# Performance work log

Measured on AMD Instinct MI355X. Metric: run time of the kernel, lower is better.

Reference implementation:

```python
import jax, jax.numpy as jnp
from jax import lax
import numpy as np

SIGMAS = (30.0, 150.0, 300.0)
RESTORE_FACTOR = 2.0
COLOR_GAIN = 10.0
GAIN = 270.0
OFFSET = 128.0
EPS = 1e-6


def _dwconv(x, k2d, stride):
    # depthwise 2D conv, NCHW, VALID padding (caller pads)
    C = x.shape[1]
    kh, kw = k2d.shape
    w = jnp.broadcast_to(k2d.astype(x.dtype)[None, None], (C, 1, kh, kw))
    return lax.conv_general_dilated(
        x, w, (stride, stride), 'VALID',
        dimension_numbers=('NCHW', 'OIHW', 'NCHW'),
        feature_group_count=C)


def _pyr_down(x):
    # cv2.pyrDown: 5x5 binomial kernel, reflect-101 border, stride-2 decimation
    k1 = jnp.array([1., 4., 6., 4., 1.], jnp.float32) / 16.0
    k2 = jnp.outer(k1, k1)
    xp = jnp.pad(x, ((0, 0), (0, 0), (2, 2), (2, 2)), mode='reflect')
    return _dwconv(xp, k2, 2)


def _gauss_blur(x, ksize):
    # cv2.GaussianBlur with sigmaX=0: sigma derived from kernel size
    s = 0.3 * ((ksize - 1) * 0.5 - 1.0) + 0.8
    i = jnp.arange(ksize, dtype=jnp.float32) - (ksize - 1) / 2.0
    g = jnp.exp(-(i * i) / (2.0 * s * s))
    g = g / g.sum()
    k2 = jnp.outer(g, g)
    p = ksize // 2
    xp = jnp.pad(x, ((0, 0), (0, 0), (p, p), (p, p)), mode='reflect')
    return _dwconv(xp, k2, 1)


def _fast_filter(x, sigma):
    # Faithful port of GaussianBlurConv.FastFilter (static Python recursion:
    # sigma is a compile-time constant, so depth is fixed at trace time).
    sigma = min(sigma, 300.0)
    k = int(round(sigma * 3 * 2 + 1)) | 1
    if k < 3:
        return x
    if k < 10:
        return _gauss_blur(x, k)
    h, w = x.shape[2], x.shape[3]
    if h < 2 or w < 2:
        return x
    sub = _fast_filter(_pyr_down(x), sigma / 2.0)
    # cv2.resize default INTER_LINEAR == half-pixel bilinear
    return jax.image.resize(sub, (x.shape[0], x.shape[1], h, w), method='bilinear')


def _msr_forward(x):
    img = x * 255.0 + 1.0                      # (N,3,H,W)
    log_img = jnp.log10(img + EPS)
    retinex = sum(log_img - jnp.log10(_fast_filter(img, s) + EPS) for s in SIGMAS)
    retinex = retinex / len(SIGMAS)
    img_sum = jnp.sum(img, axis=1, keepdims=True)   # (N,1,H,W)
    color_rest = jnp.log10(img * RESTORE_FACTOR / (img_sum + EPS) + 1.0)
    enhanced = retinex * color_rest * COLOR_GAIN * GAIN + OFFSET
    return jnp.clip(enhanced, 0.0, 255.0) / 255.0


def setup_inputs() -> dict:
    key = jax.random.key(0)
    x = jax.random.uniform(key, (8, 3, 1280, 1280), dtype=jnp.float32)
    return {"x": x}


def reference(x):
    return _msr_forward(x)
```

## Files before the change

kernel.cpp:

```cpp
#include <hip/hip_runtime.h>

#define NC 24

typedef float f32x4 __attribute__((ext_vector_type(4)));

__device__ __forceinline__ float pyr_point(const float* ip, int Hi, int Wi, int oy, int ox)
{
    const float k1[5] = {0.0625f, 0.25f, 0.375f, 0.25f, 0.0625f};
    float acc = 0.f;
#pragma unroll
    for (int i = 0; i < 5; ++i) {
        int y = 2 * oy - 2 + i;
        y = (y < 0) ? -y : y;
        y = (y >= Hi) ? (2 * Hi - 2 - y) : y;
        const float* rp = ip + (size_t)y * Wi;
        float r = 0.f;
#pragma unroll
        for (int j = 0; j < 5; ++j) {
            int xx = 2 * ox - 2 + j;
            xx = (xx < 0) ? -xx : xx;
            xx = (xx >= Wi) ? (2 * Wi - 2 - xx) : xx;
            r = fmaf(k1[j], rp[xx], r);
        }
        acc = fmaf(k1[i], r, acc);
    }
    return acc;
}

template <int K>
__device__ __forceinline__ float blur_point(const float* ip, int H, int W, int oy, int ox,
                                            const float* w)
{
    const int R = K / 2;
    float acc = 0.f;
#pragma unroll
    for (int i = 0; i < K; ++i) {
        int y = oy - R + i;
        y = (y < 0) ? -y : y;
        y = (y >= H) ? (2 * H - 2 - y) : y;
        const float* rp = ip + (size_t)y * W;
        float r = 0.f;
#pragma unroll
        for (int j = 0; j < K; ++j) {
            int xx = ox - R + j;
            xx = (xx < 0) ? -xx : xx;
            xx = (xx >= W) ? (2 * W - 2 - xx) : xx;
            r = fmaf(w[j], rp[xx], r);
        }
        acc = fmaf(w[i], r, acc);
    }
    return acc;
}

template <int HI, int WI>
__global__ void __launch_bounds__(256) pyrdown_v2(
    const float* __restrict__ in, float* __restrict__ out, float scale, float offs)
{
    const int HO = HI / 2, WO = WI / 2;
    __shared__ float tile[35][136];
    __shared__ float vs[16][132];
    const int tid = threadIdx.x;
    const int OX = blockIdx.x * 64;
    const int OY = blockIdx.y * 16;
    const int nc = blockIdx.z;
    const float k1[5] = {0.0625f, 0.25f, 0.375f, 0.25f, 0.0625f};
    const float* ip = in + (size_t)nc * HI * WI;
    const int gx0 = 2 * OX - 4;

    if (gx0 >= 0 && gx0 + 135 < WI) {
        for (int v = tid; v < 35 * 34; v += 256) {
            int r = v / 34, q = v - r * 34;
            int y = 2 * OY - 2 + r;
            y = (y < 0) ? -y : y;
            y = (y >= HI) ? (2 * HI - 2 - y) : y;
            *(f32x4*)&tile[r][4 * q] = *(const f32x4*)&ip[(size_t)y * WI + gx0 + 4 * q];
        }
    } else {
        for (int v = tid; v < 35 * 136; v += 256) {
            int r = v / 136, c = v - r * 136;
            int y = 2 * OY - 2 + r;
            y = (y < 0) ? -y : y;
            y = (y >= HI) ? (2 * HI - 2 - y) : y;
            y = min(max(y, 0), HI - 1);
            int x = gx0 + c;
            x = (x < 0) ? -x : x;
            x = (x >= WI) ? (2 * WI - 2 - x) : x;
            x = min(max(x, 0), WI - 1);
            tile[r][c] = ip[(size_t)y * WI + x];
        }
    }
    __syncthreads();

    for (int v = tid; v < 16 * 132; v += 256) {
        int r = v / 132, c = v - r * 132;
        float acc = k1[0] * tile[2 * r][c + 2];
#pragma unroll
        for (int i = 1; i < 5; ++i) acc = fmaf(k1[i], tile[2 * r + i][c + 2], acc);
        vs[r][c] = acc;
    }
    __syncthreads();

    for (int o = tid; o < 1024; o += 256) {
        int r = o >> 6, c = o & 63;
        int ox = OX + c, oy = OY + r;
        if (ox >= WO || oy >= HO) continue;
        float acc = k1[0] * vs[r][2 * c];
#pragma unroll
        for (int j = 1; j < 5; ++j) acc = fmaf(k1[j], vs[r][2 * c + j], acc);
        out[((size_t)nc * HO + oy) * WO + ox] = fmaf(acc, scale, offs);
    }
}

__global__ void __launch_bounds__(512) base_kernel(
    const float* __restrict__ L4g, float* __restrict__ b30g,
    float* __restrict__ b150g, float* __restrict__ b300g)
{
    __shared__ float sL4[80 * 80];
    __shared__ float sL5[40 * 40];
    __shared__ float sL6[20 * 20];
    __shared__ float sL7[10 * 10];
    __shared__ float sL8[5 * 5];
    const int nc = blockIdx.x;
    const int tid = threadIdx.x;

    float w7[7], w9[9];
    {
        float s = 1.4f, s2 = 2.f * s * s, sum = 0.f;
#pragma unroll
        for (int i = 0; i < 7; ++i) { float d = (float)i - 3.f; w7[i] = expf(-(d * d) / s2); sum += w7[i]; }
#pragma unroll
        for (int i = 0; i < 7; ++i) w7[i] /= sum;
        s = 1.7f; s2 = 2.f * s * s; sum = 0.f;
#pragma unroll
        for (int i = 0; i < 9; ++i) { float d = (float)i - 4.f; w9[i] = expf(-(d * d) / s2); sum += w9[i]; }
#pragma unroll
        for (int i = 0; i < 9; ++i) w9[i] /= sum;
    }

    const float* src = L4g + (size_t)nc * 6400;
    for (int i = tid; i < 1600; i += 512)
        *(f32x4*)&sL4[4 * i] = *(const f32x4*)&src[4 * i];
    __syncthreads();
    for (int i = tid; i < 1600; i += 512) {
        int oy = i / 40, ox = i - oy * 40;
        sL5[i] = pyr_point(sL4, 80, 80, oy, ox);
    }
    __syncthreads();
    for (int i = tid; i < 400; i += 512) {
        int oy = i / 20, ox = i - oy * 20;
        sL6[i] = pyr_point(sL5, 40, 40, oy, ox);
    }
    __syncthreads();
    for (int i = tid; i < 100; i += 512) {
        int oy = i / 10, ox = i - oy * 10;
        sL7[i] = pyr_point(sL6, 20, 20, oy, ox);
    }
    __syncthreads();
    for (int i = tid; i < 25; i += 512) {
        int oy = i / 5, ox = i - oy * 5;
        sL8[i] = pyr_point(sL7, 10, 10, oy, ox);
    }
    __syncthreads();
    for (int i = tid; i < 1600; i += 512) {
        int oy = i / 40, ox = i - oy * 40;
        b30g[(size_t)nc * 1600 + i] = blur_point<7>(sL5, 40, 40, oy, ox, w7);
    }
    for (int i = tid; i < 100; i += 512) {
        int oy = i / 10, ox = i - oy * 10;
        b150g[(size_t)nc * 100 + i] = blur_point<9>(sL7, 10, 10, oy, ox, w9);
    }
    for (int i = tid; i < 25; i += 512) {
        int oy = i / 5, ox = i - oy * 5;
        b300g[(size_t)nc * 25 + i] = blur_point<9>(sL8, 5, 5, oy, ox, w9);
    }
}

#define CH 1721
#define O30_3 0
#define O30_2 36
#define O30_1 100
#define O30_0 244
#define O150_5 568
#define O150_4 593
#define O150_3 618
#define O150_2 654
#define O150_1 718
#define O150_0 862
#define O300_6 1186
#define O300_5 1211
#define O300_4 1236
#define O300_3 1261
#define O300_2 1297
#define O300_1 1333
#define O300_0 1397

template <int NPL, int ND, int NS, int LSD>
__device__ __forceinline__ void up_level(float* __restrict__ S,
                                         const int (&srcO)[NPL], const int (&dstO)[NPL],
                                         int ayD, int axD, int ayS, int axS)
{
    const int SSRC = LSD / 2;
    const int NPTS = ND * ND;
    for (int pt = threadIdx.x; pt < NPTS; pt += 256) {
        int ry = pt / ND, rx = pt - ry * ND;
        int gy = min(max(ayD + ry, 0), LSD - 1);
        int gx = min(max(axD + rx, 0), LSD - 1);
        int my = gy >> 1, py = gy & 1;
        int mx = gx >> 1, px = gx & 1;
        int yA = py ? my : max(my - 1, 0);
        int yB = py ? min(my + 1, SSRC - 1) : my;
        float wyA = py ? 0.75f : 0.25f;
        float wyB = 1.0f - wyA;
        int xA = px ? mx : max(mx - 1, 0);
        int xB = px ? min(mx + 1, SSRC - 1) : mx;
        float wxA = px ? 0.75f : 0.25f;
        float wxB = 1.0f - wxA;
        int la = (yA - ayS) * NS + (xA - axS);
        int laB = la + (xB - xA);
        int lb = (yB - ayS) * NS + (xA - axS);
        int lbB = lb + (xB - xA);
#pragma unroll
        for (int p = 0; p < NPL; ++p) {
            const float* sp = S + srcO[p];
            float v = wyA * fmaf(wxA, sp[la], wxB * sp[laB]) +
                      wyB * fmaf(wxA, sp[lb], wxB * sp[lbB]);
            S[dstO[p] + pt] = v;
        }
    }
}

__global__ void __launch_bounds__(256) mega_final(
    const float* __restrict__ x,
    const float* __restrict__ b30g,
    const float* __restrict__ b150g,
    const float* __restrict__ b300g,
    float* __restrict__ out)
{
    const int H = 1280, W = 1280;
    __shared__ float S[3 * CH];

    const int tid = threadIdx.x;
    const int X0 = blockIdx.x * 64, Y0 = blockIdx.y * 64;
    const int n = blockIdx.z;

    int ay[7], ax[7];
    ay[0] = (Y0 >> 2) - 1;
    ax[0] = (X0 >> 2) - 1;
#pragma unroll
    for (int l = 1; l < 7; ++l) {
        ay[l] = (ay[l - 1] >> 1) - 1;
        ax[l] = (ax[l - 1] >> 1) - 1;
    }

    if (tid < 36) {
        int ry = tid / 6, rx = tid - ry * 6;
        int gy = min(max(ay[3] + ry, 0), 39);
        int gx = min(max(ax[3] + rx, 0), 39);
#pragma unroll
        for (int c = 0; c < 3; ++c)
            S[c * CH + O30_3 + tid] = b30g[(size_t)(n * 3 + c) * 1600 + gy * 40 + gx];
    } else if (tid >= 64 && tid < 89) {
        int t = tid - 64;
        int ry = t / 5, rx = t - ry * 5;
        int gy = min(max(ay[5] + ry, 0), 9);
        int gx = min(max(ax[5] + rx, 0), 9);
#pragma unroll
        for (int c = 0; c < 3; ++c)
            S[c * CH + O150_5 + t] = b150g[(size_t)(n * 3 + c) * 100 + gy * 10 + gx];
    } else if (tid >= 128 && tid < 153) {
        int t = tid - 128;
        int ry = t / 5, rx = t - ry * 5;
        int gy = min(max(ay[6] + ry, 0), 4);
        int gx = min(max(ax[6] + rx, 0), 4);
#pragma unroll
        for (int c = 0; c < 3; ++c)
            S[c * CH + O300_6 + t] = b300g[(size_t)(n * 3 + c) * 25 + gy * 5 + gx];
    }
    __syncthreads();

    {
        const int s[3] = {O300_6, O300_6 + CH, O300_6 + 2 * CH};
        const int d[3] = {O300_5, O300_5 + CH, O300_5 + 2 * CH};
        up_level<3, 5, 5, 10>(S, s, d, ay[5], ax[5], ay[6], ax[6]);
    }
    __syncthreads();
    {
        const int s[6] = {O300_5, O300_5 + CH, O300_5 + 2 * CH, O150_5, O150_5 + CH, O150_5 + 2 * CH};
        const int d[6] = {O300_4, O300_4 + CH, O300_4 + 2 * CH, O150_4, O150_4 + CH, O150_4 + 2 * CH};
        up_level<6, 5, 5, 20>(S, s, d, ay[4], ax[4], ay[5], ax[5]);
    }
    __syncthreads();
    {
        const int s[6] = {O300_4, O300_4 + CH, O300_4 + 2 * CH, O150_4, O150_4 + CH, O150_4 + 2 * CH};
        const int d[6] = {O300_3, O300_3 + CH, O300_3 + 2 * CH, O150_3, O150_3 + CH, O150_3 + 2 * CH};
        up_level<6, 6, 5, 40>(S, s, d, ay[3], ax[3], ay[4], ax[4]);
    }
    __syncthreads();
    {
        const int s[9] = {O300_3, O300_3 + CH, O300_3 + 2 * CH, O150_3, O150_3 + CH, O150_3 + 2 * CH,
                          O30_3, O30_3 + CH, O30_3 + 2 * CH};
        const int d[9] = {O300_2, O300_2 + CH, O300_2 + 2 * CH, O150_2, O150_2 + CH, O150_2 + 2 * CH,
                          O30_2, O30_2 + CH, O30_2 + 2 * CH};
        up_level<9, 8, 6, 80>(S, s, d, ay[2], ax[2], ay[3], ax[3]);
    }
    __syncthreads();
    {
        const int s[9] = {O300_2, O300_2 + CH, O300_2 + 2 * CH, O150_2, O150_2 + CH, O150_2 + 2 * CH,
                          O30_2, O30_2 + CH, O30_2 + 2 * CH};
        const int d[9] = {O300_1, O300_1 + CH, O300_1 + 2 * CH, O150_1, O150_1 + CH, O150_1 + 2 * CH,
                          O30_1, O30_1 + CH, O30_1 + 2 * CH};
        up_level<9, 12, 8, 160>(S, s, d, ay[1], ax[1], ay[2], ax[2]);
    }
    __syncthreads();
    {
        const int s[9] = {O300_1, O300_1 + CH, O300_1 + 2 * CH, O150_1, O150_1 + CH, O150_1 + 2 * CH,
                          O30_1, O30_1 + CH, O30_1 + 2 * CH};
        const int d[9] = {O300_0, O300_0 + CH, O300_0 + 2 * CH, O150_0, O150_0 + CH, O150_0 + 2 * CH,
                          O30_0, O30_0 + CH, O30_0 + 2 * CH};
        up_level<9, 18, 12, 320>(S, s, d, ay[0], ax[0], ay[1], ax[1]);
    }
    __syncthreads();

    int tyi = tid >> 4, txi = tid & 15;
    int byi = (Y0 >> 2) + tyi, bxi = (X0 >> 2) + txi;
    int ry[3], rx[3];
    ry[0] = max(byi - 1, 0) - ay[0]; ry[1] = byi - ay[0]; ry[2] = min(byi + 1, 319) - ay[0];
    rx[0] = max(bxi - 1, 0) - ax[0]; rx[1] = bxi - ax[0]; rx[2] = min(bxi + 1, 319) - ax[0];
    const int ol0[3] = {O30_0, O150_0, O300_0};

    f32x4 xi[3][4];
#pragma unroll
    for (int c = 0; c < 3; ++c)
#pragma unroll
        for (int qy = 0; qy < 4; ++qy)
            xi[c][qy] = __builtin_nontemporal_load(
                (const f32x4*)&x[((size_t)(n * 3 + c) * H + 4 * byi + qy) * W + 4 * bxi]);

    float crcp[4][4];
#pragma unroll
    for (int qy = 0; qy < 4; ++qy)
#pragma unroll
        for (int qx = 0; qx < 4; ++qx) {
            float s = (xi[0][qy][qx] + xi[1][qy][qx] + xi[2][qy][qx]) * 255.f + 3.f;
            crcp[qy][qx] = __fdividef(2.f, s + 1e-6f);
        }

#pragma unroll
    for (int c = 0; c < 3; ++c) {
        float prod[4][4];
#pragma unroll
        for (int qy = 0; qy < 4; ++qy)
#pragma unroll
            for (int qx = 0; qx < 4; ++qx) prod[qy][qx] = 1.f;

#pragma unroll
        for (int s = 0; s < 3; ++s) {
            const float* fp = &S[c * CH + ol0[s]];
            float v[3][3];
#pragma unroll
            for (int i = 0; i < 3; ++i)
#pragma unroll
                for (int j = 0; j < 3; ++j) v[i][j] = fp[ry[i] * 18 + rx[j]];
            float cy[4][3];
#pragma unroll
            for (int j = 0; j < 3; ++j) {
                float v0 = v[0][j], v1 = v[1][j], v2 = v[2][j];
                cy[0][j] = fmaf(0.375f, v0, 0.625f * v1);
                cy[1][j] = fmaf(0.1875f, v0, fmaf(0.75f, v1, 0.0625f * v2));
                cy[2][j] = fmaf(0.0625f, v0, fmaf(0.75f, v1, 0.1875f * v2));
                cy[3][j] = fmaf(0.625f, v1, 0.375f * v2);
            }
#pragma unroll
            for (int qy = 0; qy < 4; ++qy) {
                float a0 = cy[qy][0], a1 = cy[qy][1], a2 = cy[qy][2];
                float t0 = fmaf(0.375f, a0, 0.625f * a1);
                float t1 = fmaf(0.1875f, a0, fmaf(0.75f, a1, 0.0625f * a2));
                float t2 = fmaf(0.0625f, a0, fmaf(0.75f, a1, 0.1875f * a2));
                float t3 = fmaf(0.625f, a1, 0.375f * a2);
                prod[qy][0] *= (t0 + 1e-6f);
                prod[qy][1] *= (t1 + 1e-6f);
                prod[qy][2] *= (t2 + 1e-6f);
                prod[qy][3] *= (t3 + 1e-6f);
            }
        }

#pragma unroll
        for (int qy = 0; qy < 4; ++qy) {
            f32x4 o;
#pragma unroll
            for (int qx = 0; qx < 4; ++qx) {
                float img = xi[c][qy][qx] * 255.f + 1.f;
                float a = img + 1e-6f;
                float l2a = __log2f(__fdividef(a * a * a, prod[qy][qx]));
                float carg = fmaf(img, crcp[qy][qx], 1.f);
                float l2c = __log2f(carg);
                float e = fmaf(l2a * l2c, 81.55715246f, 128.f);
                e = fminf(fmaxf(e, 0.f), 255.f);
                o[qx] = e * (1.f / 255.f);
            }
            __builtin_nontemporal_store(
                o, (f32x4*)&out[((size_t)(n * 3 + c) * H + 4 * byi + qy) * W + 4 * bxi]);
        }
    }
}

extern "C" void kernel_launch(void* const* d_in, const int* in_sizes, int n_in,
                              void* d_out, int out_size, void* d_ws, size_t ws_size,
                              hipStream_t stream)
{
    const float* x = (const float*)d_in[0];
    float* out = (float*)d_out;
    float* ws = (float*)d_ws;

    size_t off = 0;
    auto alloc = [&](int d) { float* p = ws + off; off += (size_t)NC * d * d; return p; };
    float* L1 = alloc(640);
    float* L2 = alloc(320);
    float* L3 = alloc(160);
    float* L4 = alloc(80);
    float* b30 = alloc(40);
    float* b150 = alloc(10);
    float* b300 = alloc(5);
    (void)ws_size; (void)in_sizes; (void)n_in; (void)out_size;

    dim3 blk(256, 1, 1);

    pyrdown_v2<1280, 1280><<<dim3(10, 40, NC), blk, 0, stream>>>(x,  L1, 255.f, 1.f);
    pyrdown_v2<640, 640><<<dim3(5, 20, NC), blk, 0, stream>>>(L1, L2, 1.f, 0.f);
    pyrdown_v2<320, 320><<<dim3(3, 10, NC), blk, 0, stream>>>(L2, L3, 1.f, 0.f);
    pyrdown_v2<160, 160><<<dim3(2, 5, NC), blk, 0, stream>>>(L3, L4, 1.f, 0.f);
    base_kernel<<<dim3(NC, 1, 1), dim3(512, 1, 1), 0, stream>>>(L4, b30, b150, b300);
    mega_final<<<dim3(20, 20, 8), dim3(256, 1, 1), 0, stream>>>(x, b30, b150, b300, out);
}
```

Baseline: 351.5 us.

## Collapse cascaded bilinear upsampling into precomputed separable 3-tap weights

The chain of per-level bilinear upsample stages in shared memory, each followed by a barrier, is replaced by a direct mapping from a 3x3 coarse-level neighbourhood to each output pixel. The mapping uses separable weights that are computed per row and column once per block by composing the linear interpolation steps. This removes six barriers and the intermediate shared-memory levels, and shrinks the shared-memory footprint. In exchange each thread does more FMAs per pixel, loads weights from shared memory, and keeps more live registers (prod for all three channels). Accuracy relies on the composed weights matching the clamped border behaviour of the original cascade.

```diff
diff --git a/kernel.cpp b/kernel.cpp
--- a/kernel.cpp
+++ b/kernel.cpp
@@ -175,60 +175,6 @@
     }
 }
 
-#define CH 1721
-#define O30_3 0
-#define O30_2 36
-#define O30_1 100
-#define O30_0 244
-#define O150_5 568
-#define O150_4 593
-#define O150_3 618
-#define O150_2 654
-#define O150_1 718
-#define O150_0 862
-#define O300_6 1186
-#define O300_5 1211
-#define O300_4 1236
-#define O300_3 1261
-#define O300_2 1297
-#define O300_1 1333
-#define O300_0 1397
-
-template <int NPL, int ND, int NS, int LSD>
-__device__ __forceinline__ void up_level(float* __restrict__ S,
-                                         const int (&srcO)[NPL], const int (&dstO)[NPL],
-                                         int ayD, int axD, int ayS, int axS)
-{
-    const int SSRC = LSD / 2;
-    const int NPTS = ND * ND;
-    for (int pt = threadIdx.x; pt < NPTS; pt += 256) {
-        int ry = pt / ND, rx = pt - ry * ND;
-        int gy = min(max(ayD + ry, 0), LSD - 1);
-        int gx = min(max(axD + rx, 0), LSD - 1);
-        int my = gy >> 1, py = gy & 1;
-        int mx = gx >> 1, px = gx & 1;
-        int yA = py ? my : max(my - 1, 0);
-        int yB = py ? min(my + 1, SSRC - 1) : my;
-        float wyA = py ? 0.75f : 0.25f;
-        float wyB = 1.0f - wyA;
-        int xA = px ? mx : max(mx - 1, 0);
-        int xB = px ? min(mx + 1, SSRC - 1) : mx;
-        float wxA = px ? 0.75f : 0.25f;
-        float wxB = 1.0f - wxA;
-        int la = (yA - ayS) * NS + (xA - axS);
-        int laB = la + (xB - xA);
-        int lb = (yB - ayS) * NS + (xA - axS);
-        int lbB = lb + (xB - xA);
-#pragma unroll
-        for (int p = 0; p < NPL; ++p) {
-            const float* sp = S + srcO[p];
-            float v = wyA * fmaf(wxA, sp[la], wxB * sp[laB]) +
-                      wyB * fmaf(wxA, sp[lb], wxB * sp[lbB]);
-            S[dstO[p] + pt] = v;
-        }
-    }
-}
-
 __global__ void __launch_bounds__(256) mega_final(
     const float* __restrict__ x,
     const float* __restrict__ b30g,
@@ -237,96 +183,104 @@
     float* __restrict__ out)
 {
     const int H = 1280, W = 1280;
-    __shared__ float S[3 * CH];
+    __shared__ float W30[32][3];
+    __shared__ float W150[128][3];
+    __shared__ float W300[256][3];
+    __shared__ float P30[3][4][4];
+    __shared__ float P150[3][3][3];
+    __shared__ float P300[3][3][3];
 
     const int tid = threadIdx.x;
-    const int X0 = blockIdx.x * 64, Y0 = blockIdx.y * 64;
-    const int n = blockIdx.z;
-
-    int ay[7], ax[7];
-    ay[0] = (Y0 >> 2) - 1;
-    ax[0] = (X0 >> 2) - 1;
-#pragma unroll
-    for (int l = 1; l < 7; ++l) {
-        ay[l] = (ay[l - 1] >> 1) - 1;
-        ax[l] = (ax[l - 1] >> 1) - 1;
-    }
-
-    if (tid < 36) {
-        int ry = tid / 6, rx = tid - ry * 6;
-        int gy = min(max(ay[3] + ry, 0), 39);
-        int gx = min(max(ax[3] + rx, 0), 39);
-#pragma unroll
-        for (int c = 0; c < 3; ++c)
-            S[c * CH + O30_3 + tid] = b30g[(size_t)(n * 3 + c) * 1600 + gy * 40 + gx];
-    } else if (tid >= 64 && tid < 89) {
-        int t = tid - 64;
-        int ry = t / 5, rx = t - ry * 5;
-        int gy = min(max(ay[5] + ry, 0), 9);
-        int gx = min(max(ax[5] + rx, 0), 9);
-#pragma unroll
-        for (int c = 0; c < 3; ++c)
-            S[c * CH + O150_5 + t] = b150g[(size_t)(n * 3 + c) * 100 + gy * 10 + gx];
-    } else if (tid >= 128 && tid < 153) {
-        int t = tid - 128;
-        int ry = t / 5, rx = t - ry * 5;
-        int gy = min(max(ay[6] + ry, 0), 4);
-        int gx = min(max(ax[6] + rx, 0), 4);
-#pragma unroll
-        for (int c = 0; c < 3; ++c)
-            S[c * CH + O300_6 + t] = b300g[(size_t)(n * 3 + c) * 25 + gy * 5 + gx];
-    }
-    __syncthreads();
+    const int bx = blockIdx.x, by = blockIdx.y, n = blockIdx.z;
+
+    for (int r = tid; r < 416; r += 256) {
+        int idx, nst; float* dst;
+        if (r < 32)       { idx = r;       nst = 5; dst = W30[r]; }
+        else if (r < 160) { idx = r - 32;  nst = 7; dst = W150[r - 32]; }
+        else              { idx = r - 160; nst = 8; dst = W300[r - 160]; }
+        float w0 = 0.f, w1 = 1.f, w2 = 0.f;
+        for (int k = 0; k < nst; ++k) {
+            int c = (idx >> k) & 1;
+            float a0 = c ? 0.25f * w0 : fmaf(0.75f, w0, 0.25f * w1);
+            float a1 = c ? fmaf(0.75f, w0, fmaf(0.75f, w1, 0.25f * w2))
+                         : fmaf(0.25f, w0, fmaf(0.75f, w1, 0.75f * w2));
+            float a2 = c ? fmaf(0.25f, w1, 0.75f * w2) : 0.25f * w2;
+            w0 = a0; w1 = a1; w2 = a2;
+        }
+        dst[0] = w0; dst[1] = w1; dst[2] = w2;
+    }
 
     {
-        const int s[3] = {O300_6, O300_6 + CH, O300_6 + 2 * CH};
-        const int d[3] = {O300_5, O300_5 + CH, O300_5 + 2 * CH};
-        up_level<3, 5, 5, 10>(S, s, d, ay[5], ax[5], ay[6], ax[6]);
-    }
-    __syncthreads();
-    {
-        const int s[6] = {O300_5, O300_5 + CH, O300_5 + 2 * CH, O150_5, O150_5 + CH, O150_5 + 2 * CH};
-        const int d[6] = {O300_4, O300_4 + CH, O300_4 + 2 * CH, O150_4, O150_4 + CH, O150_4 + 2 * CH};
-        up_level<6, 5, 5, 20>(S, s, d, ay[4], ax[4], ay[5], ax[5]);
-    }
-    __syncthreads();
-    {
-        const int s[6] = {O300_4, O300_4 + CH, O300_4 + 2 * CH, O150_4, O150_4 + CH, O150_4 + 2 * CH};
-        const int d[6] = {O300_3, O300_3 + CH, O300_3 + 2 * CH, O150_3, O150_3 + CH, O150_3 + 2 * CH};
-        up_level<6, 6, 5, 40>(S, s, d, ay[3], ax[3], ay[4], ax[4]);
-    }
-    __syncthreads();
-    {
-        const int s[9] = {O300_3, O300_3 + CH, O300_3 + 2 * CH, O150_3, O150_3 + CH, O150_3 + 2 * CH,
-                          O30_3, O30_3 + CH, O30_3 + 2 * CH};
-        const int d[9] = {O300_2, O300_2 + CH, O300_2 + 2 * CH, O150_2, O150_2 + CH, O150_2 + 2 * CH,
-                          O30_2, O30_2 + CH, O30_2 + 2 * CH};
-        up_level<9, 8, 6, 80>(S, s, d, ay[2], ax[2], ay[3], ax[3]);
-    }
-    __syncthreads();
-    {
-        const int s[9] = {O300_2, O300_2 + CH, O300_2 + 2 * CH, O150_2, O150_2 + CH, O150_2 + 2 * CH,
-                          O30_2, O30_2 + CH, O30_2 + 2 * CH};
-        const int d[9] = {O300_1, O300_1 + CH, O300_1 + 2 * CH, O150_1, O150_1 + CH, O150_1 + 2 * CH,
-                          O30_1, O30_1 + CH, O30_1 + 2 * CH};
-        up_level<9, 12, 8, 160>(S, s, d, ay[1], ax[1], ay[2], ax[2]);
-    }
-    __syncthreads();
-    {
-        const int s[9] = {O300_1, O300_1 + CH, O300_1 + 2 * CH, O150_1, O150_1 + CH, O150_1 + 2 * CH,
-                          O30_1, O30_1 + CH, O30_1 + 2 * CH};
-        const int d[9] = {O300_0, O300_0 + CH, O300_0 + 2 * CH, O150_0, O150_0 + CH, O150_0 + 2 * CH,
-                          O30_0, O30_0 + CH, O30_0 + 2 * CH};
-        up_level<9, 18, 12, 320>(S, s, d, ay[0], ax[0], ay[1], ax[1]);
-    }
-    __syncthreads();
-
-    int tyi = tid >> 4, txi = tid & 15;
-    int byi = (Y0 >> 2) + tyi, bxi = (X0 >> 2) + txi;
-    int ry[3], rx[3];
-    ry[0] = max(byi - 1, 0) - ay[0]; ry[1] = byi - ay[0]; ry[2] = min(byi + 1, 319) - ay[0];
-    rx[0] = max(bxi - 1, 0) - ax[0]; rx[1] = bxi - ax[0]; rx[2] = min(bxi + 1, 319) - ax[0];
-    const int ol0[3] = {O30_0, O150_0, O300_0};
+        const int ay30 = 2 * by - 1, ax30 = 2 * bx - 1;
+        const int ay150 = (by >> 1) - 1, ax150 = (bx >> 1) - 1;
+        const int ay300 = (by >> 2) - 1, ax300 = (bx >> 2) - 1;
+        for (int i = tid; i < 48; i += 256) {
+            int c = i >> 4, j = i & 15, ry = j >> 2, rx = j & 3;
+            int gy = min(max(ay30 + ry, 0), 39), gx = min(max(ax30 + rx, 0), 39);
+            P30[c][ry][rx] = b30g[(size_t)(n * 3 + c) * 1600 + gy * 40 + gx];
+        }
+        for (int i = tid; i < 27; i += 256) {
+            int c = i / 9, j = i - 9 * c, ry = j / 3, rx = j - 3 * ry;
+            int gy = min(max(ay150 + ry, 0), 9), gx = min(max(ax150 + rx, 0), 9);
+            P150[c][ry][rx] = b150g[(size_t)(n * 3 + c) * 100 + gy * 10 + gx];
+        }
+        for (int i = tid; i < 27; i += 256) {
+            int c = i / 9, j = i - 9 * c, ry = j / 3, rx = j - 3 * ry;
+            int gy = min(max(ay300 + ry, 0), 4), gx = min(max(ax300 + rx, 0), 4);
+            P300[c][ry][rx] = b300g[(size_t)(n * 3 + c) * 25 + gy * 5 + gx];
+        }
+    }
+    __syncthreads();
+
+    const int tyi = tid >> 4, txi = tid & 15;
+    const int byi = 16 * by + tyi, bxi = 16 * bx + txi;
+    const int sy30 = tyi >> 3, sx30 = txi >> 3;
+    const int ryb[3] = {(4 * tyi) & 31, 64 * (by & 1) + 4 * tyi, 64 * (by & 3) + 4 * tyi};
+    const int rxb[3] = {(4 * txi) & 31, 64 * (bx & 1) + 4 * txi, 64 * (bx & 3) + 4 * txi};
+
+    float prod[4][4][3];
+#pragma unroll
+    for (int qy = 0; qy < 4; ++qy)
+#pragma unroll
+        for (int qx = 0; qx < 4; ++qx)
+#pragma unroll
+            for (int c = 0; c < 3; ++c) prod[qy][qx][c] = 1.f;
+
+#pragma unroll
+    for (int s = 0; s < 3; ++s) {
+        float wy[4][3], wx[4][3];
+#pragma unroll
+        for (int q = 0; q < 4; ++q) {
+#pragma unroll
+            for (int i = 0; i < 3; ++i) {
+                wy[q][i] = (s == 0) ? W30[ryb[0] + q][i]
+                         : (s == 1) ? W150[ryb[1] + q][i] : W300[ryb[2] + q][i];
+                wx[q][i] = (s == 0) ? W30[rxb[0] + q][i]
+                         : (s == 1) ? W150[rxb[1] + q][i] : W300[rxb[2] + q][i];
+            }
+        }
+#pragma unroll
+        for (int c = 0; c < 3; ++c) {
+            float v[3][3];
+#pragma unroll
+            for (int i = 0; i < 3; ++i)
+#pragma unroll
+                for (int j = 0; j < 3; ++j)
+                    v[i][j] = (s == 0) ? P30[c][sy30 + i][sx30 + j]
+                            : (s == 1) ? P150[c][i][j] : P300[c][i][j];
+#pragma unroll
+            for (int qy = 0; qy < 4; ++qy) {
+                float c0 = fmaf(wy[qy][0], v[0][0], fmaf(wy[qy][1], v[1][0], wy[qy][2] * v[2][0]));
+                float c1 = fmaf(wy[qy][0], v[0][1], fmaf(wy[qy][1], v[1][1], wy[qy][2] * v[2][1]));
+                float c2 = fmaf(wy[qy][0], v[0][2], fmaf(wy[qy][1], v[1][2], wy[qy][2] * v[2][2]));
+#pragma unroll
+                for (int qx = 0; qx < 4; ++qx) {
+                    float val = fmaf(wx[qx][0], c0, fmaf(wx[qx][1], c1, wx[qx][2] * c2));
+                    prod[qy][qx][c] *= (val + 1e-6f);
+                }
+            }
+        }
+    }
 
     f32x4 xi[3][4];
 #pragma unroll
@@ -347,43 +301,6 @@
 
 #pragma unroll
     for (int c = 0; c < 3; ++c) {
-        float prod[4][4];
-#pragma unroll
-        for (int qy = 0; qy < 4; ++qy)
-#pragma unroll
-            for (int qx = 0; qx < 4; ++qx) prod[qy][qx] = 1.f;
-
-#pragma unroll
-        for (int s = 0; s < 3; ++s) {
-            const float* fp = &S[c * CH + ol0[s]];
-            float v[3][3];
-#pragma unroll
-            for (int i = 0; i < 3; ++i)
-#pragma unroll
-                for (int j = 0; j < 3; ++j) v[i][j] = fp[ry[i] * 18 + rx[j]];
-            float cy[4][3];
-#pragma unroll
-            for (int j = 0; j < 3; ++j) {
-                float v0 = v[0][j], v1 = v[1][j], v2 = v[2][j];
-                cy[0][j] = fmaf(0.375f, v0, 0.625f * v1);
-                cy[1][j] = fmaf(0.1875f, v0, fmaf(0.75f, v1, 0.0625f * v2));
-                cy[2][j] = fmaf(0.0625f, v0, fmaf(0.75f, v1, 0.1875f * v2));
-                cy[3][j] = fmaf(0.625f, v1, 0.375f * v2);
-            }
-#pragma unroll
-            for (int qy = 0; qy < 4; ++qy) {
-                float a0 = cy[qy][0], a1 = cy[qy][1], a2 = cy[qy][2];
-                float t0 = fmaf(0.375f, a0, 0.625f * a1);
-                float t1 = fmaf(0.1875f, a0, fmaf(0.75f, a1, 0.0625f * a2));
-                float t2 = fmaf(0.0625f, a0, fmaf(0.75f, a1, 0.1875f * a2));
-                float t3 = fmaf(0.625f, a1, 0.375f * a2);
-                prod[qy][0] *= (t0 + 1e-6f);
-                prod[qy][1] *= (t1 + 1e-6f);
-                prod[qy][2] *= (t2 + 1e-6f);
-                prod[qy][3] *= (t3 + 1e-6f);
-            }
-        }
-
 #pragma unroll
         for (int qy = 0; qy < 4; ++qy) {
             f32x4 o;
@@ -391,7 +308,7 @@
             for (int qx = 0; qx < 4; ++qx) {
                 float img = xi[c][qy][qx] * 255.f + 1.f;
                 float a = img + 1e-6f;
-                float l2a = __log2f(__fdividef(a * a * a, prod[qy][qx]));
+                float l2a = __log2f(__fdividef(a * a * a, prod[qy][qx][c]));
                 float carg = fmaf(img, crcp[qy][qx], 1.f);
                 float l2c = __log2f(carg);
                 float e = fmaf(l2a * l2c, 81.55715246f, 128.f);
```

Result: slower. 358.8 us (+2.1%).
